# Optimization experiments

Measured on AMD Instinct MI355X. Metric: run time of the kernel, lower is better.

The kernel has to match this reference:

```python
import jax, jax.numpy as jnp
import numpy as np

B, S, DIM = 2, 2048, 2048
H, KVH = 16, 8
HD = DIM // H            # 128
WIN = 512                # sliding window size
GLOB = 64                # global tokens
NEG = -1000000000.0


def _alibi_slopes(n):
    cp2 = 2.0 ** jnp.floor(jnp.log2(jnp.float32(n)))
    base = 2.0 ** (-(2.0 ** (-(jnp.log2(cp2) - 3.0))))
    powers = jnp.arange(1, 1 + n, dtype=jnp.float32)
    return jnp.power(base, powers)  # [n]


def _rope_tables(head_dim, seq_len, dtype=jnp.float32, base=10000.0):
    half = head_dim // 2
    freqs = 1.0 / base ** (jnp.arange(0, half, dtype=dtype) / half)
    t = jnp.arange(seq_len, dtype=dtype)
    f = jnp.outer(t, freqs)                       # [S, half]
    return jnp.sin(f)[None, None], jnp.cos(f)[None, None]  # [1,1,S,half]


def _rotary(x, sin, cos):
    # x: [b,h,s,d]; nonstandard rotation per source module
    x1, x2 = jnp.split(x, 2, axis=-1)
    return jnp.concatenate([x1 * cos - x2 * sin, x1 * sin + x2 * cos], axis=-1)


def _window_mask(seq_len):
    # Faithful to create_sliding_window_mask: 0.0 inside window / global rows+cols, -1e9 elsewhere
    i = jnp.arange(seq_len)[:, None]
    j = jnp.arange(seq_len)[None, :]
    m = jnp.where(jnp.abs(i - j) <= WIN // 2, 0.0, NEG)
    m = jnp.where((i < GLOB) | (j < GLOB), 0.0, m)
    return m  # [S, S] float


def setup_inputs() -> dict:
    key = jax.random.key(0)
    k1, k2, k3, k4 = jax.random.split(key, 4)
    x = jax.random.normal(k1, (B, S, DIM), dtype=jnp.float32)
    Wq = jax.random.normal(k2, (DIM, DIM), dtype=jnp.float32) * 0.02
    Wkv = jax.random.normal(k3, (DIM, 2 * KVH * HD), dtype=jnp.float32) * 0.02
    Wo = jax.random.normal(k4, (DIM, DIM), dtype=jnp.float32) * 0.02
    bo = jnp.zeros((DIM,), dtype=jnp.float32)
    return {"x": x, "Wq": Wq, "Wkv": Wkv, "Wo": Wo, "bo": bo}


def reference(x, Wq, Wkv, Wo, bo):
    b, s, dim = x.shape
    # token-complexity gating on queries
    complexity = jax.nn.sigmoid(jnp.sum(jnp.abs(x), axis=-1, keepdims=True))  # [b,s,1]
    q = jnp.dot(x * complexity, Wq)       # [b,s,dim]
    kv = jnp.dot(x, Wkv)                  # [b,s,2*kv_dim]
    k, v = jnp.split(kv, 2, axis=-1)

    q = q.reshape(b, s, H, HD).transpose(0, 2, 1, 3)      # [b,H,s,d]
    k = k.reshape(b, s, KVH, HD).transpose(0, 2, 1, 3)    # [b,KVH,s,d]
    v = v.reshape(b, s, KVH, HD).transpose(0, 2, 1, 3)

    sin, cos = _rope_tables(HD, s, dtype=x.dtype)
    q = _rotary(q, sin, cos)
    k = _rotary(k, sin, cos)

    r = H // KVH
    k = jnp.repeat(k, r, axis=1)   # 'b h s d -> b (h r) s d'
    v = jnp.repeat(v, r, axis=1)

    scale = 1.0 / jnp.sqrt(jnp.float32(HD)).astype(x.dtype)
    qk = jnp.einsum('bhid,bhjd->bhij', q, k) * scale      # [b,H,s,s]

    # ALiBi bias
    slopes = _alibi_slopes(H)                             # [H]
    pos = jnp.arange(s)
    dist = -jnp.abs(pos[:, None] - pos[None, :]).astype(jnp.float32)  # [s,s]
    qk = qk + slopes[:, None, None] * dist                # broadcast over batch

    # Faithful to source: jnp.where(float_mask, qk, NEG) treats nonzero (-1e9,
    # i.e. OUTSIDE window) as True -> keeps qk; zero (inside window) -> NEG.
    m = _window_mask(s)
    qk = jnp.where(m != 0.0, qk, NEG)

    attn = jax.nn.softmax(qk, axis=-1)
    out = jnp.einsum('bhij,bhjd->bhid', attn, v)          # [b,H,s,d]
    out = out.transpose(0, 2, 1, 3).reshape(b, s, dim)
    out = jnp.dot(out, Wo) + bo
    return out
```

## Files before the change

kernel.cpp:

```cpp
#include <hip/hip_runtime.h>

#define DEVI static __device__ __forceinline__

typedef __attribute__((ext_vector_type(8))) short short8;
typedef __attribute__((ext_vector_type(4))) short short4v;
typedef __attribute__((ext_vector_type(4))) float f32x4;

DEVI float bf2f(short u) {
  union { unsigned u32; float f; } c;
  c.u32 = ((unsigned)(unsigned short)u) << 16;
  return c.f;
}
DEVI short f2bf(float f) {
  union { float f; unsigned u32; } c; c.f = f;
  unsigned x = c.u32;
  unsigned r = (x + 0x7FFFu + ((x >> 16) & 1u)) >> 16;
  return (short)(unsigned short)r;
}
DEVI float ex2(float x) {
  float r;
  asm("v_exp_f32 %0, %1" : "=v"(r) : "v"(x));
  return r;
}
DEVI unsigned cvtpk(float lo, float hi) {
  unsigned r;
  asm("v_cvt_pk_bf16_f32 %0, %1, %2" : "=v"(r) : "v"(lo), "v"(hi));
  return r;
}

DEVI void gload16(const void* g, void* l) {
  __builtin_amdgcn_global_load_lds(
      (__attribute__((address_space(1))) void*)(g),
      (__attribute__((address_space(3))) void*)(l), 16, 0, 0);
}

#define LOG2E 1.4426950408889634f
#define QSCALE 0.1275174470974102f

__global__ void prep_kernel(const float* __restrict__ x, short* __restrict__ xq,
                            short* __restrict__ xb, float* __restrict__ tsin,
                            float* __restrict__ tcos,
                            const float* __restrict__ Wq, const float* __restrict__ Wkv,
                            const float* __restrict__ Wo, short* __restrict__ T0,
                            short* __restrict__ T1, short* __restrict__ T2) {
  __shared__ float red[4];
  __shared__ __align__(16) short tile[64][68];
  const int bid = blockIdx.x, t = threadIdx.x;
  if (bid < 4096) {
    int row = bid;
    const float4* xr = (const float4*)(x + (size_t)row * 2048);
    float4 v0 = xr[t], v1 = xr[t + 256];
    float s = fabsf(v0.x) + fabsf(v0.y) + fabsf(v0.z) + fabsf(v0.w)
            + fabsf(v1.x) + fabsf(v1.y) + fabsf(v1.z) + fabsf(v1.w);
#pragma unroll
    for (int m = 1; m < 64; m <<= 1) s += __shfl_xor(s, m, 64);
    if ((t & 63) == 0) red[t >> 6] = s;
    __syncthreads();
    float tot = red[0] + red[1] + red[2] + red[3];
    float sc = 1.0f / (1.0f + expf(-tot));
    short4v q0, q1, b0, b1;
    q0[0] = f2bf(v0.x * sc); q0[1] = f2bf(v0.y * sc); q0[2] = f2bf(v0.z * sc); q0[3] = f2bf(v0.w * sc);
    q1[0] = f2bf(v1.x * sc); q1[1] = f2bf(v1.y * sc); q1[2] = f2bf(v1.z * sc); q1[3] = f2bf(v1.w * sc);
    b0[0] = f2bf(v0.x); b0[1] = f2bf(v0.y); b0[2] = f2bf(v0.z); b0[3] = f2bf(v0.w);
    b1[0] = f2bf(v1.x); b1[1] = f2bf(v1.y); b1[2] = f2bf(v1.z); b1[3] = f2bf(v1.w);
    size_t base = (size_t)row * 512;
    ((short4v*)xq)[base + t]       = q0;
    ((short4v*)xq)[base + t + 256] = q1;
    ((short4v*)xb)[base + t]       = b0;
    ((short4v*)xb)[base + t + 256] = b1;
  } else if (bid < 4608) {
    int idx = (bid - 4096) * 256 + t;
    int d = idx >> 11, s2 = idx & 2047;
    float freq = powf(10000.0f, -(float)d / 64.0f);
    float f = (float)s2 * freq;
    tsin[idx] = sinf(f);
    tcos[idx] = cosf(f);
  } else {
    int wt = bid - 4608;
    const float* W = (wt < 1024) ? Wq : (wt < 2048 ? Wkv : Wo);
    short* WT      = (wt < 1024) ? T0 : (wt < 2048 ? T1 : T2);
    int n0 = (wt & 31) * 64, k0 = ((wt >> 5) & 31) * 64;
    int tr = t >> 4, tc = t & 15;
#pragma unroll
    for (int p = 0; p < 4; ++p) {
      int r = p * 16 + tr;
      int c = tc * 4;
      float4 v = *(const float4*)&W[(size_t)(k0 + r) * 2048 + n0 + c];
      tile[c + 0][r] = f2bf(v.x);
      tile[c + 1][r] = f2bf(v.y);
      tile[c + 2][r] = f2bf(v.z);
      tile[c + 3][r] = f2bf(v.w);
    }
    __syncthreads();
#pragma unroll
    for (int p = 0; p < 4; ++p) {
      int n = p * 16 + tr;
      int c = tc * 4;
      *(short4v*)&WT[(size_t)(n0 + n) * 2048 + k0 + c] = *(const short4v*)&tile[n][c];
    }
  }
}

DEVI void gemm_core(const short* __restrict__ A, const short* __restrict__ BT,
                    int K, int m0, int n0, int tid,
                    short* As0, short* As1, short* Bs0, short* Bs1,
                    f32x4 (&acc)[2][8]) {
  const int wid = tid >> 6, lane = tid & 63;
  const int l15 = lane & 15, l4 = lane >> 4;
  const int sw7 = l15 & 7;
  const int T = K >> 6;
  auto STAGE = [&](short* Asb, short* Bsb, int t) {
#pragma unroll
    for (int p = 0; p < 4; ++p) {
      int cid = p * 256 + tid;
      int row = cid >> 3, ch = cid & 7;
      int cole = (ch ^ (row & 7)) * 8;
      gload16(A + (size_t)(m0 + row) * K + t * 64 + cole, Asb + cid * 8);
      gload16(BT + (size_t)(n0 + row) * K + t * 64 + cole, Bsb + cid * 8);
    }
  };
  STAGE(As0, Bs0, 0);
  for (int t = 0; t < T; ++t) {
    short* Asc = (t & 1) ? As1 : As0;
    short* Bsc = (t & 1) ? Bs1 : Bs0;
    if (t + 1 < T) {
      STAGE((t & 1) ? As0 : As1, (t & 1) ? Bs0 : Bs1, t + 1);
      asm volatile("s_waitcnt vmcnt(8)" ::: "memory");
    } else {
      asm volatile("s_waitcnt vmcnt(0)" ::: "memory");
    }
    __builtin_amdgcn_s_barrier();
#pragma unroll
    for (int kk = 0; kk < 2; ++kk) {
      const int cc = ((kk * 4 + l4) ^ sw7) * 8;
      short8 af0 = *(const short8*)&Asc[(wid * 32 + l15) * 64 + cc];
      short8 af1 = *(const short8*)&Asc[(wid * 32 + 16 + l15) * 64 + cc];
      short8 bf0 = *(const short8*)&Bsc[(0 * 16 + l15) * 64 + cc];
      short8 bf1 = *(const short8*)&Bsc[(1 * 16 + l15) * 64 + cc];
      short8 bf2 = *(const short8*)&Bsc[(2 * 16 + l15) * 64 + cc];
      short8 bf3 = *(const short8*)&Bsc[(3 * 16 + l15) * 64 + cc];
      __builtin_amdgcn_s_setprio(1);
      acc[0][0] = __builtin_amdgcn_mfma_f32_16x16x32_bf16(af0, bf0, acc[0][0], 0, 0, 0);
      acc[1][0] = __builtin_amdgcn_mfma_f32_16x16x32_bf16(af1, bf0, acc[1][0], 0, 0, 0);
      acc[0][1] = __builtin_amdgcn_mfma_f32_16x16x32_bf16(af0, bf1, acc[0][1], 0, 0, 0);
      acc[1][1] = __builtin_amdgcn_mfma_f32_16x16x32_bf16(af1, bf1, acc[1][1], 0, 0, 0);
      acc[0][2] = __builtin_amdgcn_mfma_f32_16x16x32_bf16(af0, bf2, acc[0][2], 0, 0, 0);
      acc[1][2] = __builtin_amdgcn_mfma_f32_16x16x32_bf16(af1, bf2, acc[1][2], 0, 0, 0);
      acc[0][3] = __builtin_amdgcn_mfma_f32_16x16x32_bf16(af0, bf3, acc[0][3], 0, 0, 0);
      acc[1][3] = __builtin_amdgcn_mfma_f32_16x16x32_bf16(af1, bf3, acc[1][3], 0, 0, 0);
      __builtin_amdgcn_s_setprio(0);
      bf0 = *(const short8*)&Bsc[(4 * 16 + l15) * 64 + cc];
      bf1 = *(const short8*)&Bsc[(5 * 16 + l15) * 64 + cc];
      bf2 = *(const short8*)&Bsc[(6 * 16 + l15) * 64 + cc];
      bf3 = *(const short8*)&Bsc[(7 * 16 + l15) * 64 + cc];
      __builtin_amdgcn_s_setprio(1);
      acc[0][4] = __builtin_amdgcn_mfma_f32_16x16x32_bf16(af0, bf0, acc[0][4], 0, 0, 0);
      acc[1][4] = __builtin_amdgcn_mfma_f32_16x16x32_bf16(af1, bf0, acc[1][4], 0, 0, 0);
      acc[0][5] = __builtin_amdgcn_mfma_f32_16x16x32_bf16(af0, bf1, acc[0][5], 0, 0, 0);
      acc[1][5] = __builtin_amdgcn_mfma_f32_16x16x32_bf16(af1, bf1, acc[1][5], 0, 0, 0);
      acc[0][6] = __builtin_amdgcn_mfma_f32_16x16x32_bf16(af0, bf2, acc[0][6], 0, 0, 0);
      acc[1][6] = __builtin_amdgcn_mfma_f32_16x16x32_bf16(af1, bf2, acc[1][6], 0, 0, 0);
      acc[0][7] = __builtin_amdgcn_mfma_f32_16x16x32_bf16(af0, bf3, acc[0][7], 0, 0, 0);
      acc[1][7] = __builtin_amdgcn_mfma_f32_16x16x32_bf16(af1, bf3, acc[1][7], 0, 0, 0);
      __builtin_amdgcn_s_setprio(0);
    }
    __builtin_amdgcn_s_barrier();
  }
}

__launch_bounds__(256, 2)
__global__ void gemm_qkv_kernel(const short* __restrict__ xq, const short* __restrict__ WqT,
                                const short* __restrict__ xb, const short* __restrict__ WkvT,
                                short* __restrict__ qr, short* __restrict__ kr,
                                short* __restrict__ vt,
                                const float* __restrict__ tsin, const float* __restrict__ tcos) {
  __shared__ __align__(16) short As[2][128 * 64];
  __shared__ __align__(16) short Bs[2][128 * 64];
  const int which = blockIdx.z;
  const int tid = threadIdx.x;
  const int nb = gridDim.x * gridDim.y;
  const int orig = blockIdx.y * gridDim.x + blockIdx.x;
  const int swz = (orig & 7) * (nb >> 3) + (orig >> 3);
  const int m0 = (swz / gridDim.x) * 128, n0 = (swz % gridDim.x) * 128;
  const short* A  = which ? xb : xq;
  const short* BT = which ? WkvT : WqT;
  f32x4 acc[2][8] = {};
  gemm_core(A, BT, 2048, m0, n0, tid, &As[0][0], &As[1][0], &Bs[0][0], &Bs[1][0], acc);

  const int wid = tid >> 6, lane = tid & 63;
  const int l15 = lane & 15, l4 = lane >> 4;
  const int b = m0 >> 11;
  const int sb = (m0 & 2047) + wid * 32;
  if (which == 0) {
    const int h = n0 >> 7;
    const size_t obase = ((size_t)(b * 16 + h) * 2048 + sb) * 128;
#pragma unroll
    for (int mi = 0; mi < 2; ++mi) {
      int srel = sb + mi * 16 + l4 * 4;
#pragma unroll
      for (int ni = 0; ni < 4; ++ni) {
        int d = ni * 16 + l15;
        float4 sn = *(const float4*)&tsin[d * 2048 + srel];
        float4 cs = *(const float4*)&tcos[d * 2048 + srel];
#pragma unroll
        for (int r = 0; r < 4; ++r) {
          float x1 = acc[mi][ni][r], x2 = acc[mi][ni + 4][r];
          float snr = (&sn.x)[r], csr = (&cs.x)[r];
          size_t ro = obase + (size_t)(mi * 16 + l4 * 4 + r) * 128;
          qr[ro + d]      = f2bf((x1 * csr - x2 * snr) * QSCALE);
          qr[ro + d + 64] = f2bf((x1 * snr + x2 * csr) * QSCALE);
        }
      }
    }
  } else {
    if (n0 < 1024) {
      const int kvh = n0 >> 7;
      const size_t obase = ((size_t)(b * 8 + kvh) * 2048 + sb) * 128;
#pragma unroll
      for (int mi = 0; mi < 2; ++mi) {
        int srel = sb + mi * 16 + l4 * 4;
#pragma unroll
        for (int ni = 0; ni < 4; ++ni) {
          int d = ni * 16 + l15;
          float4 sn = *(const float4*)&tsin[d * 2048 + srel];
          float4 cs = *(const float4*)&tcos[d * 2048 + srel];
#pragma unroll
          for (int r = 0; r < 4; ++r) {
            float x1 = acc[mi][ni][r], x2 = acc[mi][ni + 4][r];
            float snr = (&sn.x)[r], csr = (&cs.x)[r];
            size_t ro = obase + (size_t)(mi * 16 + l4 * 4 + r) * 128;
            kr[ro + d]      = f2bf(x1 * csr - x2 * snr);
            kr[ro + d + 64] = f2bf(x1 * snr + x2 * csr);
          }
        }
      }
    } else {
      const int kvh = (n0 - 1024) >> 7;
      const size_t vb = (size_t)(b * 8 + kvh) * 128;
#pragma unroll
      for (int mi = 0; mi < 2; ++mi) {
        int srel = sb + mi * 16 + l4 * 4;
#pragma unroll
        for (int ni = 0; ni < 8; ++ni) {
          int d = ni * 16 + l15;
          uint2 w;
          w.x = cvtpk(acc[mi][ni][0], acc[mi][ni][1]);
          w.y = cvtpk(acc[mi][ni][2], acc[mi][ni][3]);
          *(uint2*)&vt[(vb + d) * 2048 + srel] = w;
        }
      }
    }
  }
}

__launch_bounds__(256, 2)
__global__ void gemm_out_kernel(const short* __restrict__ A, const short* __restrict__ BT,
                                float* __restrict__ Cout, const float* __restrict__ bias) {
  __shared__ __align__(16) short As[2][128 * 64];
  __shared__ __align__(16) short Bs[2][128 * 64];
  const int tid = threadIdx.x;
  const int nb = gridDim.x * gridDim.y;
  const int orig = blockIdx.y * gridDim.x + blockIdx.x;
  const int swz = (orig & 7) * (nb >> 3) + (orig >> 3);
  const int m0 = (swz / gridDim.x) * 128, n0 = (swz % gridDim.x) * 128;
  f32x4 acc[2][8] = {};
  gemm_core(A, BT, 2048, m0, n0, tid, &As[0][0], &As[1][0], &Bs[0][0], &Bs[1][0], acc);
  const int wid = tid >> 6, lane = tid & 63;
  const int l15 = lane & 15, l4 = lane >> 4;
#pragma unroll
  for (int mi = 0; mi < 2; ++mi) {
#pragma unroll
    for (int ni = 0; ni < 8; ++ni) {
      int col = n0 + ni * 16 + l15;
      float badd = bias[col];
#pragma unroll
      for (int r = 0; r < 4; ++r) {
        int row = m0 + wid * 32 + mi * 16 + l4 * 4 + r;
        Cout[(size_t)row * 2048 + col] = acc[mi][ni][r] + badd;
      }
    }
  }
}

__launch_bounds__(512, 4)
__global__ void attn_kernel(const short* __restrict__ qr, const short* __restrict__ kr,
                            const short* __restrict__ vt, short* __restrict__ ob) {
  __shared__ __align__(16) short Ks[2][64 * 128];
  __shared__ __align__(16) short Vs[2][128 * 64];
  __shared__ __align__(16) short PL[8][16 * 64];
  const int tid = threadIdx.x;
  const int wid = tid >> 6, lane = tid & 63;
  const int l15 = lane & 15, l4 = lane >> 4;
  const int sw7 = l15 & 7;
  const int l4h = l4 >> 1, l4l = l4 & 1;
  const int f = blockIdx.x + (blockIdx.y << 4) + (blockIdx.z << 8);
  const int swb = (f & 7) * 64 + (f >> 3);
  const int qt = swb & 15, h = (swb >> 4) & 15, b = swb >> 8;
  const int kh = h >> 1;
  const int qb = qt * 128;
  const int q0 = qb + wid * 16;
  const float slope2 = exp2f(-0.5f * (float)(h + 1)) * LOG2E;
  const size_t qbase = ((size_t)(b * 16 + h) * 2048 + q0) * 128;
  const size_t kbase = ((size_t)(b * 8 + kh) * 2048) * 128;
  const size_t vbase = ((size_t)(b * 8 + kh) * 128) * 2048;
  short* pl = PL[wid];

  short8 aq[4];
#pragma unroll
  for (int kk = 0; kk < 4; ++kk)
    aq[kk] = *(const short8*)&qr[qbase + (size_t)l15 * 128 + kk * 32 + l4 * 8];

  f32x4 o[8] = {};
  float m_run = -1e30f, l_run = 0.0f;
  const int iq = q0 + l15;

  int lo0, n0t, lo1, n1t;
  if (qt == 0)      { lo0 = 0;   n0t = 32;          lo1 = 0; n1t = 0; }
  else if (qt == 1) { lo0 = 384; n0t = 26;          lo1 = 0; n1t = 0; }
  else {
    lo0 = 64;        n0t = 2 * qt - 3;
    lo1 = qb + 256;  n1t = (28 - 2 * qt > 0) ? (28 - 2 * qt) : 0;
  }
  const int nt = n0t + n1t;
  auto KV0 = [&](int i) { return i < n0t ? lo0 + i * 64 : lo1 + (i - n0t) * 64; };

  auto STAGE = [&](int bi, int kv0) {
#pragma unroll
    for (int i2 = 0; i2 < 2; ++i2) {
      int cid = i2 * 512 + tid;
      int krow = cid >> 4, kch = cid & 15;
      gload16(kr + kbase + (size_t)(kv0 + krow) * 128 + ((kch ^ (krow & 7)) * 8),
              &Ks[bi][cid * 8]);
    }
#pragma unroll
    for (int i2 = 0; i2 < 2; ++i2) {
      int cid = i2 * 512 + tid;
      int vrow = cid >> 3, vch = cid & 7;
      gload16(vt + vbase + (size_t)vrow * 2048 + kv0 + ((vch ^ (vrow & 7)) * 8),
              &Vs[bi][cid * 8]);
    }
  };

  STAGE(0, KV0(0));
  __syncthreads();
  int cur = 0;

  for (int it = 0; it < nt; ++it) {
    const int kv0 = KV0(it);
    if (it + 1 < nt) STAGE(cur ^ 1, KV0(it + 1));

    int mode;
    if (q0 + 15 < 64 || kv0 == 0) mode = 3;
    else if (kv0 <= q0 - 320)     mode = 1;
    else if (kv0 >= q0 + 272)     mode = 2;
    else                          mode = 0;

    if (mode != 3) {
      f32x4 sc[4];
#pragma unroll
      for (int jj = 0; jj < 4; ++jj) sc[jj] = (f32x4){0.f, 0.f, 0.f, 0.f};
      __builtin_amdgcn_s_setprio(1);
#pragma unroll
      for (int kk = 0; kk < 4; ++kk) {
#pragma unroll
        for (int jj = 0; jj < 4; ++jj) {
          short8 bk = *(const short8*)&Ks[cur][(jj * 16 + l15) * 128 + (((kk * 4 + l4) ^ sw7) * 8)];
          sc[jj] = __builtin_amdgcn_mfma_f32_16x16x32_bf16(bk, aq[kk], sc[jj], 0, 0, 0);
        }
      }
      __builtin_amdgcn_s_setprio(0);
      float pm = -1e30f;
      const float dbase = (float)(iq - kv0 - l4 * 4);
      if (mode == 0) {
#pragma unroll
        for (int jj = 0; jj < 4; ++jj) {
          float dj = dbase - 16.0f * jj;
#pragma unroll
          for (int r = 0; r < 4; ++r) {
            float d = dj - (float)r;
            float ad = fabsf(d);
            float v = fmaf(-slope2, ad, sc[jj][r]);
            v = (ad > 256.0f) ? v : -1e9f;
            sc[jj][r] = v;
            pm = fmaxf(pm, v);
          }
        }
      } else {
        const float sl = (mode == 1) ? -slope2 : slope2;
#pragma unroll
        for (int jj = 0; jj < 4; ++jj) {
          float dj = dbase - 16.0f * jj;
#pragma unroll
          for (int r = 0; r < 4; ++r) {
            float v = fmaf(sl, dj - (float)r, sc[jj][r]);
            sc[jj][r] = v;
            pm = fmaxf(pm, v);
          }
        }
      }
      pm = fmaxf(pm, __shfl_xor(pm, 16, 64));
      pm = fmaxf(pm, __shfl_xor(pm, 32, 64));
      if (!__all(pm <= m_run + 8.0f)) {
        float mn = fmaxf(m_run, pm);
        float corr = ex2(m_run - mn);
        l_run *= corr;
#pragma unroll
        for (int dn = 0; dn < 8; ++dn)
#pragma unroll
          for (int r = 0; r < 4; ++r) o[dn][r] *= corr;
        m_run = mn;
      }
      float psum = 0.0f;
#pragma unroll
      for (int jj = 0; jj < 2; ++jj) {
        float p0 = ex2(sc[jj][0] - m_run), p1 = ex2(sc[jj][1] - m_run);
        float p2 = ex2(sc[jj][2] - m_run), p3 = ex2(sc[jj][3] - m_run);
        psum += (p0 + p1) + (p2 + p3);
        uint2 w; w.x = cvtpk(p0, p1); w.y = cvtpk(p2, p3);
        *(uint2*)&pl[l15 * 64 + (((jj * 2 + l4h) ^ sw7) * 8) + l4l * 4] = w;
      }
      asm volatile("s_waitcnt lgkmcnt(0)" ::: "memory");
      __builtin_amdgcn_sched_barrier(0);
      short8 pa = *(const short8*)&pl[l15 * 64 + ((l4 ^ sw7) * 8)];
      short8 bv0[8];
#pragma unroll
      for (int dn = 0; dn < 8; ++dn)
        bv0[dn] = *(const short8*)&Vs[cur][(dn * 16 + l15) * 64 + ((l4 ^ sw7) * 8)];
      uint2 w2[2];
#pragma unroll
      for (int jj = 2; jj < 4; ++jj) {
        float p0 = ex2(sc[jj][0] - m_run), p1 = ex2(sc[jj][1] - m_run);
        float p2 = ex2(sc[jj][2] - m_run), p3 = ex2(sc[jj][3] - m_run);
        psum += (p0 + p1) + (p2 + p3);
        w2[jj - 2].x = cvtpk(p0, p1); w2[jj - 2].y = cvtpk(p2, p3);
      }
      __builtin_amdgcn_s_setprio(1);
#pragma unroll
      for (int dn = 0; dn < 8; ++dn)
        o[dn] = __builtin_amdgcn_mfma_f32_16x16x32_bf16(bv0[dn], pa, o[dn], 0, 0, 0);
      __builtin_amdgcn_s_setprio(0);
#pragma unroll
      for (int jj = 2; jj < 4; ++jj)
        *(uint2*)&pl[l15 * 64 + (((jj * 2 + l4h) ^ sw7) * 8) + l4l * 4] = w2[jj - 2];
      asm volatile("s_waitcnt lgkmcnt(0)" ::: "memory");
      __builtin_amdgcn_sched_barrier(0);
      pa = *(const short8*)&pl[l15 * 64 + (((4 + l4) ^ sw7) * 8)];
      __builtin_amdgcn_s_setprio(1);
#pragma unroll
      for (int dn = 0; dn < 8; ++dn) {
        short8 bv = *(const short8*)&Vs[cur][(dn * 16 + l15) * 64 + (((4 + l4) ^ sw7) * 8)];
        o[dn] = __builtin_amdgcn_mfma_f32_16x16x32_bf16(bv, pa, o[dn], 0, 0, 0);
      }
      __builtin_amdgcn_s_setprio(0);
      psum += __shfl_xor(psum, 16, 64);
      psum += __shfl_xor(psum, 32, 64);
      l_run += psum;
    } else {
      float pm = -1e9f;
      if (!__all(pm <= m_run + 8.0f)) {
        float mn = fmaxf(m_run, pm);
        float corr = ex2(m_run - mn);
        l_run *= corr;
#pragma unroll
        for (int dn = 0; dn < 8; ++dn)
#pragma unroll
          for (int r = 0; r < 4; ++r) o[dn][r] *= corr;
        m_run = mn;
      }
      float pu = ex2(-1e9f - m_run);
      l_run += 64.0f * pu;
      unsigned uu = cvtpk(pu, pu);
      short8 pa;
      ((unsigned*)&pa)[0] = uu; ((unsigned*)&pa)[1] = uu;
      ((unsigned*)&pa)[2] = uu; ((unsigned*)&pa)[3] = uu;
      __builtin_amdgcn_s_setprio(1);
#pragma unroll
      for (int c = 0; c < 2; ++c) {
#pragma unroll
        for (int dn = 0; dn < 8; ++dn) {
          short8 bv = *(const short8*)&Vs[cur][(dn * 16 + l15) * 64 + (((c * 4 + l4) ^ sw7) * 8)];
          o[dn] = __builtin_amdgcn_mfma_f32_16x16x32_bf16(bv, pa, o[dn], 0, 0, 0);
        }
      }
      __builtin_amdgcn_s_setprio(0);
    }
    __syncthreads();
    cur ^= 1;
  }

  float inv = 1.0f / l_run;
  size_t rbase = ((size_t)(b * 2048 + iq) * 16 + h) * 128;
#pragma unroll
  for (int dn = 0; dn < 8; ++dn) {
    uint2 w;
    w.x = cvtpk(o[dn][0] * inv, o[dn][1] * inv);
    w.y = cvtpk(o[dn][2] * inv, o[dn][3] * inv);
    *(uint2*)&ob[rbase + dn * 16 + l4 * 4] = w;
  }
}

extern "C" void kernel_launch(void* const* d_in, const int* in_sizes, int n_in,
                              void* d_out, int out_size, void* d_ws, size_t ws_size,
                              hipStream_t stream) {
  const float* x   = (const float*)d_in[0];
  const float* Wq  = (const float*)d_in[1];
  const float* Wkv = (const float*)d_in[2];
  const float* Wo  = (const float*)d_in[3];
  const float* bo  = (const float*)d_in[4];
  float* out = (float*)d_out;

  char* ws = (char*)d_ws;
  size_t off = 0;
  auto alloc = [&](size_t bytes) -> void* {
    void* p = ws + off;
    off += (bytes + 255) & ~(size_t)255;
    return p;
  };
  float* tsin  = (float*)alloc(64 * 2048 * 4);
  float* tcos  = (float*)alloc(64 * 2048 * 4);
  short* WqT   = (short*)alloc((size_t)2048 * 2048 * 2);
  short* WkvT  = (short*)alloc((size_t)2048 * 2048 * 2);
  short* WoT   = (short*)alloc((size_t)2048 * 2048 * 2);
  short* xq    = (short*)alloc((size_t)4096 * 2048 * 2);
  short* xb    = (short*)alloc((size_t)4096 * 2048 * 2);
  short* qr    = (short*)alloc((size_t)2 * 16 * 2048 * 128 * 2);
  short* kr    = (short*)alloc((size_t)2 * 8 * 2048 * 128 * 2);
  short* vt    = (short*)alloc((size_t)2 * 8 * 2048 * 128 * 2);
  short* ob    = xq;

  prep_kernel<<<7680, 256, 0, stream>>>(x, xq, xb, tsin, tcos, Wq, Wkv, Wo, WqT, WkvT, WoT);
  gemm_qkv_kernel<<<dim3(16, 32, 2), 256, 0, stream>>>(xq, WqT, xb, WkvT, qr, kr, vt, tsin, tcos);
  attn_kernel<<<dim3(16, 16, 2), 512, 0, stream>>>(qr, kr, vt, ob);
  gemm_out_kernel<<<dim3(16, 32), 256, 0, stream>>>(ob, WoT, out, bo);
  (void)in_sizes; (void)n_in; (void)out_size; (void)ws_size;
}
```

Before: 229.6 us.

## Apply query gating scale in QKV epilogue and simplify PV softmax pipeline

The per-row sigmoid gating factor is now stored as one float per token and applied in the Q projection epilogue, using linearity of the matmul. This drops the separate scaled bf16 copy of x, so both GEMM halves read the same A matrix and one 16 MB write is removed from prep. Separately, the attention PV loop is restructured: all four exp/pack steps finish before two MFMA chunks run, replacing the earlier interleaved software pipeline. That may reduce overlap between exp and MFMA but cuts LDS waits. Rounding now happens after scaling, so numerics differ slightly.

```diff
diff --git a/kernel.cpp b/kernel.cpp
--- a/kernel.cpp
+++ b/kernel.cpp
@@ -37,8 +37,8 @@
 #define LOG2E 1.4426950408889634f
 #define QSCALE 0.1275174470974102f
 
-__global__ void prep_kernel(const float* __restrict__ x, short* __restrict__ xq,
-                            short* __restrict__ xb, float* __restrict__ tsin,
+__global__ void prep_kernel(const float* __restrict__ x, short* __restrict__ xb,
+                            float* __restrict__ scale, float* __restrict__ tsin,
                             float* __restrict__ tcos,
                             const float* __restrict__ Wq, const float* __restrict__ Wkv,
                             const float* __restrict__ Wo, short* __restrict__ T0,
@@ -56,16 +56,14 @@
     for (int m = 1; m < 64; m <<= 1) s += __shfl_xor(s, m, 64);
     if ((t & 63) == 0) red[t >> 6] = s;
     __syncthreads();
-    float tot = red[0] + red[1] + red[2] + red[3];
-    float sc = 1.0f / (1.0f + expf(-tot));
-    short4v q0, q1, b0, b1;
-    q0[0] = f2bf(v0.x * sc); q0[1] = f2bf(v0.y * sc); q0[2] = f2bf(v0.z * sc); q0[3] = f2bf(v0.w * sc);
-    q1[0] = f2bf(v1.x * sc); q1[1] = f2bf(v1.y * sc); q1[2] = f2bf(v1.z * sc); q1[3] = f2bf(v1.w * sc);
+    if (t == 0) {
+      float tot = red[0] + red[1] + red[2] + red[3];
+      scale[row] = 1.0f / (1.0f + expf(-tot));
+    }
+    short4v b0, b1;
     b0[0] = f2bf(v0.x); b0[1] = f2bf(v0.y); b0[2] = f2bf(v0.z); b0[3] = f2bf(v0.w);
     b1[0] = f2bf(v1.x); b1[1] = f2bf(v1.y); b1[2] = f2bf(v1.z); b1[3] = f2bf(v1.w);
     size_t base = (size_t)row * 512;
-    ((short4v*)xq)[base + t]       = q0;
-    ((short4v*)xq)[base + t + 256] = q1;
     ((short4v*)xb)[base + t]       = b0;
     ((short4v*)xb)[base + t + 256] = b1;
   } else if (bid < 4608) {
@@ -169,8 +167,8 @@
 }
 
 __launch_bounds__(256, 2)
-__global__ void gemm_qkv_kernel(const short* __restrict__ xq, const short* __restrict__ WqT,
-                                const short* __restrict__ xb, const short* __restrict__ WkvT,
+__global__ void gemm_qkv_kernel(const short* __restrict__ xb, const short* __restrict__ WqT,
+                                const short* __restrict__ WkvT, const float* __restrict__ scale,
                                 short* __restrict__ qr, short* __restrict__ kr,
                                 short* __restrict__ vt,
                                 const float* __restrict__ tsin, const float* __restrict__ tcos) {
@@ -182,10 +180,9 @@
   const int orig = blockIdx.y * gridDim.x + blockIdx.x;
   const int swz = (orig & 7) * (nb >> 3) + (orig >> 3);
   const int m0 = (swz / gridDim.x) * 128, n0 = (swz % gridDim.x) * 128;
-  const short* A  = which ? xb : xq;
   const short* BT = which ? WkvT : WqT;
   f32x4 acc[2][8] = {};
-  gemm_core(A, BT, 2048, m0, n0, tid, &As[0][0], &As[1][0], &Bs[0][0], &Bs[1][0], acc);
+  gemm_core(xb, BT, 2048, m0, n0, tid, &As[0][0], &As[1][0], &Bs[0][0], &Bs[1][0], acc);
 
   const int wid = tid >> 6, lane = tid & 63;
   const int l15 = lane & 15, l4 = lane >> 4;
@@ -197,6 +194,7 @@
 #pragma unroll
     for (int mi = 0; mi < 2; ++mi) {
       int srel = sb + mi * 16 + l4 * 4;
+      float4 scv = *(const float4*)&scale[m0 + wid * 32 + mi * 16 + l4 * 4];
 #pragma unroll
       for (int ni = 0; ni < 4; ++ni) {
         int d = ni * 16 + l15;
@@ -204,11 +202,12 @@
         float4 cs = *(const float4*)&tcos[d * 2048 + srel];
 #pragma unroll
         for (int r = 0; r < 4; ++r) {
+          float qs = QSCALE * (&scv.x)[r];
           float x1 = acc[mi][ni][r], x2 = acc[mi][ni + 4][r];
           float snr = (&sn.x)[r], csr = (&cs.x)[r];
           size_t ro = obase + (size_t)(mi * 16 + l4 * 4 + r) * 128;
-          qr[ro + d]      = f2bf((x1 * csr - x2 * snr) * QSCALE);
-          qr[ro + d + 64] = f2bf((x1 * snr + x2 * csr) * QSCALE);
+          qr[ro + d]      = f2bf((x1 * csr - x2 * snr) * qs);
+          qr[ro + d + 64] = f2bf((x1 * snr + x2 * csr) * qs);
         }
       }
     }
@@ -412,49 +411,32 @@
       }
       float psum = 0.0f;
 #pragma unroll
-      for (int jj = 0; jj < 2; ++jj) {
-        float p0 = ex2(sc[jj][0] - m_run), p1 = ex2(sc[jj][1] - m_run);
-        float p2 = ex2(sc[jj][2] - m_run), p3 = ex2(sc[jj][3] - m_run);
+      for (int jj = 0; jj < 4; ++jj) {
+        float p0 = ex2(sc[jj][0] - m_run);
+        float p1 = ex2(sc[jj][1] - m_run);
+        float p2 = ex2(sc[jj][2] - m_run);
+        float p3 = ex2(sc[jj][3] - m_run);
         psum += (p0 + p1) + (p2 + p3);
         uint2 w; w.x = cvtpk(p0, p1); w.y = cvtpk(p2, p3);
-        *(uint2*)&pl[l15 * 64 + (((jj * 2 + l4h) ^ sw7) * 8) + l4l * 4] = w;
-      }
-      asm volatile("s_waitcnt lgkmcnt(0)" ::: "memory");
-      __builtin_amdgcn_sched_barrier(0);
-      short8 pa = *(const short8*)&pl[l15 * 64 + ((l4 ^ sw7) * 8)];
-      short8 bv0[8];
-#pragma unroll
-      for (int dn = 0; dn < 8; ++dn)
-        bv0[dn] = *(const short8*)&Vs[cur][(dn * 16 + l15) * 64 + ((l4 ^ sw7) * 8)];
-      uint2 w2[2];
-#pragma unroll
-      for (int jj = 2; jj < 4; ++jj) {
-        float p0 = ex2(sc[jj][0] - m_run), p1 = ex2(sc[jj][1] - m_run);
-        float p2 = ex2(sc[jj][2] - m_run), p3 = ex2(sc[jj][3] - m_run);
-        psum += (p0 + p1) + (p2 + p3);
-        w2[jj - 2].x = cvtpk(p0, p1); w2[jj - 2].y = cvtpk(p2, p3);
-      }
-      __builtin_amdgcn_s_setprio(1);
-#pragma unroll
-      for (int dn = 0; dn < 8; ++dn)
-        o[dn] = __builtin_amdgcn_mfma_f32_16x16x32_bf16(bv0[dn], pa, o[dn], 0, 0, 0);
-      __builtin_amdgcn_s_setprio(0);
-#pragma unroll
-      for (int jj = 2; jj < 4; ++jj)
-        *(uint2*)&pl[l15 * 64 + (((jj * 2 + l4h) ^ sw7) * 8) + l4l * 4] = w2[jj - 2];
-      asm volatile("s_waitcnt lgkmcnt(0)" ::: "memory");
-      __builtin_amdgcn_sched_barrier(0);
-      pa = *(const short8*)&pl[l15 * 64 + (((4 + l4) ^ sw7) * 8)];
-      __builtin_amdgcn_s_setprio(1);
-#pragma unroll
-      for (int dn = 0; dn < 8; ++dn) {
-        short8 bv = *(const short8*)&Vs[cur][(dn * 16 + l15) * 64 + (((4 + l4) ^ sw7) * 8)];
-        o[dn] = __builtin_amdgcn_mfma_f32_16x16x32_bf16(bv, pa, o[dn], 0, 0, 0);
-      }
-      __builtin_amdgcn_s_setprio(0);
+        int ad = l15 * 64 + (((jj * 2 + l4h) ^ sw7) * 8) + l4l * 4;
+        *(uint2*)&pl[ad] = w;
+      }
       psum += __shfl_xor(psum, 16, 64);
       psum += __shfl_xor(psum, 32, 64);
       l_run += psum;
+      asm volatile("s_waitcnt lgkmcnt(0)" ::: "memory");
+      __builtin_amdgcn_sched_barrier(0);
+      __builtin_amdgcn_s_setprio(1);
+#pragma unroll
+      for (int c = 0; c < 2; ++c) {
+        short8 pa = *(const short8*)&pl[l15 * 64 + (((c * 4 + l4) ^ sw7) * 8)];
+#pragma unroll
+        for (int dn = 0; dn < 8; ++dn) {
+          short8 bv = *(const short8*)&Vs[cur][(dn * 16 + l15) * 64 + (((c * 4 + l4) ^ sw7) * 8)];
+          o[dn] = __builtin_amdgcn_mfma_f32_16x16x32_bf16(bv, pa, o[dn], 0, 0, 0);
+        }
+      }
+      __builtin_amdgcn_s_setprio(0);
     } else {
       float pm = -1e9f;
       if (!__all(pm <= m_run + 8.0f)) {
@@ -518,18 +500,18 @@
   };
   float* tsin  = (float*)alloc(64 * 2048 * 4);
   float* tcos  = (float*)alloc(64 * 2048 * 4);
+  float* scale = (float*)alloc(4096 * 4);
   short* WqT   = (short*)alloc((size_t)2048 * 2048 * 2);
   short* WkvT  = (short*)alloc((size_t)2048 * 2048 * 2);
   short* WoT   = (short*)alloc((size_t)2048 * 2048 * 2);
-  short* xq    = (short*)alloc((size_t)4096 * 2048 * 2);
   short* xb    = (short*)alloc((size_t)4096 * 2048 * 2);
   short* qr    = (short*)alloc((size_t)2 * 16 * 2048 * 128 * 2);
   short* kr    = (short*)alloc((size_t)2 * 8 * 2048 * 128 * 2);
   short* vt    = (short*)alloc((size_t)2 * 8 * 2048 * 128 * 2);
-  short* ob    = xq;
-
-  prep_kernel<<<7680, 256, 0, stream>>>(x, xq, xb, tsin, tcos, Wq, Wkv, Wo, WqT, WkvT, WoT);
-  gemm_qkv_kernel<<<dim3(16, 32, 2), 256, 0, stream>>>(xq, WqT, xb, WkvT, qr, kr, vt, tsin, tcos);
+  short* ob    = xb;
+
+  prep_kernel<<<7680, 256, 0, stream>>>(x, xb, scale, tsin, tcos, Wq, Wkv, Wo, WqT, WkvT, WoT);
+  gemm_qkv_kernel<<<dim3(16, 32, 2), 256, 0, stream>>>(xb, WqT, WkvT, scale, qr, kr, vt, tsin, tcos);
   attn_kernel<<<dim3(16, 16, 2), 512, 0, stream>>>(qr, kr, vt, ob);
   gemm_out_kernel<<<dim3(16, 32), 256, 0, stream>>>(ob, WoT, out, bo);
   (void)in_sizes; (void)n_in; (void)out_size; (void)ws_size;
```

Result: faster. 220.5 us, median of 2 (-4.0%).
